# Kernel tuning notes

Hardware: AMD Instinct MI355X
Metric: run time of the kernel (lower is better)

## Reference

```python
import jax, jax.numpy as jnp
import numpy as np


def setup_inputs() -> dict:
    key = jax.random.key(0)
    ks = jax.random.split(key, 6)
    m, d, n, p = 4096, 1024, 16, 1024  # tokens, input_dim, num_experts, output_dim (=slots)
    h = (d + p) * 2 // 3  # 1365, hidden_dim per original module
    s = 0.02
    return {
        "x": jax.random.normal(ks[0], (m, d), jnp.float32),
        "phi": jax.random.normal(ks[1], (d, n, p), jnp.float32) * s,
        "W1": jax.random.normal(ks[2], (n, d, h), jnp.float32) * s,
        "b1": jax.random.normal(ks[3], (n, h), jnp.float32) * s,
        "W2": jax.random.normal(ks[4], (n, h, p), jnp.float32) * s,
        "b2": jax.random.normal(ks[5], (n, p), jnp.float32) * s,
    }


def reference(x, phi, W1, b1, W2, b2):
    # logits: [m, n, p] = tokens x experts x slots
    logits = jnp.einsum('md,dnp->mnp', x, phi)
    # Dispatch weights: softmax over tokens' expert axis (dim=1 in torch == experts n)
    D = jax.nn.softmax(logits, axis=1)
    # Combine weights: softmax over all (expert, slot) pairs per token
    m = logits.shape[0]
    C = jax.nn.softmax(logits.reshape(m, -1), axis=-1).reshape(logits.shape)
    # Slot inputs: [n, p, d]
    Xs = jnp.einsum('md,mnp->npd', x, D)
    # Batched per-expert MLP (replaces the Python loop over experts)
    H = jax.nn.relu(jnp.einsum('npd,ndh->nph', Xs, W1) + b1[:, None, :])
    Ys = jnp.einsum('nph,nho->npo', H, W2) + b2[:, None, :]  # [n, p, out]
    # Combine: [m, out]; flatten(start_dim=1) on a 2D tensor is a no-op
    Y = jnp.einsum('npo,mnp->mo', Ys, C)
    return Y
```

## Files before the change

### kernel.cpp

```cpp
#include <hip/hip_runtime.h>
#include <math.h>

#define MTOK 4096
#define DDIM 1024
#define NEXP 16
#define PSLOT 1024
#define NPDIM 16384
#define HDIM 1365
#define HPAD 1376
#define KSPL 4

typedef unsigned short u16;
typedef __attribute__((ext_vector_type(8))) short short8;
typedef __attribute__((ext_vector_type(8))) unsigned short ushort8;
typedef __attribute__((ext_vector_type(2))) unsigned int uint32x2;
typedef __attribute__((ext_vector_type(4))) unsigned int uint32x4;
typedef __attribute__((ext_vector_type(4))) float f32x4;

template<bool Bc, typename T, typename F> struct cond_t { using type = T; };
template<typename T, typename F> struct cond_t<false, T, F> { using type = F; };

__device__ __forceinline__ float b2f(u16 v) {
    union { unsigned int u; float f; } x;
    x.u = ((unsigned int)v) << 16;
    return x.f;
}
__device__ __forceinline__ u16 f2b(float f) {
    union { float f; unsigned int u; } x;
    x.f = f;
    unsigned int r = x.u + 0x7FFFu + ((x.u >> 16) & 1u);
    return (u16)(r >> 16);
}
__device__ __forceinline__ unsigned int cvtpk(float lo, float hi) {
    unsigned int r;
    asm("v_cvt_pk_bf16_f32 %0, %1, %2" : "=v"(r) : "v"(lo), "v"(hi));
    return r;
}
__device__ __forceinline__ void stv(float* p, long long i, float v) { p[i] = v; }
__device__ __forceinline__ void stv(u16*  p, long long i, float v) { p[i] = f2b(v); }

template<int AMODE, typename TA, typename TB, typename TC,
         bool BIASF, bool RELUF, bool ROWSC, bool BCHK>
__global__ __launch_bounds__(512) void mgemm(
    const TA* __restrict__ A, long long sA, int lda,
    const TB* __restrict__ B, long long sB, int ldb,
    TC* __restrict__ C, long long sC, int ldc,
    const float* __restrict__ S,
    const float* __restrict__ bias, long long sBias,
    const float* __restrict__ rowsc,
    int M, int N, int NZ, int K, int Kb, int Nb)
{
    constexpr int AS = (AMODE == 0) ? 32 : 40;
    constexpr int BS = 40;
    __shared__ u16 As[2][256 * AS];
    __shared__ u16 Bs[2][128 * BS];

    const int bz = blockIdx.z;
    A += (long long)bz * sA;
    B += (long long)bz * sB;
    C += (long long)bz * sC;
    const float* biasp = BIASF ? (bias + (long long)bz * sBias) : nullptr;

    const int gx = gridDim.x;
    const int nwg = gx * gridDim.y;
    int wg = blockIdx.x + gx * blockIdx.y;
    {
        const int q = nwg >> 3, r = nwg & 7, xc = wg & 7, ix = wg >> 3;
        wg = (xc < r ? xc * (q + 1) : r + xc * q) + ix;
    }
    const int m0 = (wg / gx) * 256;
    const int n0 = (wg % gx) * 128;

    const int tid  = threadIdx.x;
    const int lane = tid & 63;
    const int wv   = tid >> 6;
    const int wm   = wv & 3;
    const int wn   = wv >> 2;
    const int quad = lane >> 4;
    const int l16  = lane & 15;

    const int cla  = 2 * (tid & 127);
    const int k8a  = tid >> 7;
    const int clb  = 2 * (tid & 63);
    const int kqb  = tid >> 6;
    const int ngb  = n0 + clb;

    auto aoff = [&](int row, int k8) {
        int o = row * AS + k8 * 8;
        if constexpr (AMODE != 0) o ^= ((row >> 3) & 3) << 3;
        return o;
    };
    auto boff = [&](int row, int kel) {
        return (row * BS + kel) ^ (((row >> 3) & 3) << 3);
    };

    f32x4 acc[4][4];
#pragma unroll
    for (int i = 0; i < 4; ++i)
#pragma unroll
        for (int j = 0; j < 4; ++j) acc[i][j] = (f32x4){0.f, 0.f, 0.f, 0.f};

    using BRAW = typename cond_t<sizeof(TB) == 2, unsigned int[4], float[8]>::type;

    auto LOADA = [&](int k0, int buf, unsigned int (&araw)[8], float2 (&sr)[8]) {
        if constexpr (AMODE == 0) {
#pragma unroll
            for (int q = 0; q < 2; ++q) {
                const u16* gp = A + (long long)(m0 + wv * 32 + q * 16 + (lane >> 2)) * lda
                                  + k0 + (lane & 3) * 8;
                u16* lp = &As[buf][(wv * 32 + q * 16) * 32];
                __builtin_amdgcn_global_load_lds(
                    (const __attribute__((address_space(1))) unsigned int*)gp,
                    (__attribute__((address_space(3))) unsigned int*)lp, 16, 0, 0);
            }
        } else {
#pragma unroll
            for (int i = 0; i < 8; ++i) {
                const long long kg = k0 + k8a * 8 + i;
                araw[i] = *(const unsigned int*)((const u16*)A + kg * lda + (m0 + cla));
                sr[i]   = *(const float2*)&S[kg * 1024 + ((m0 + cla) & 1023)];
            }
        }
    };
    auto WRITEA = [&](int buf, unsigned int (&araw)[8], float2 (&sr)[8]) {
        if constexpr (AMODE != 0) {
            uint32x4 wa, wb;
#pragma unroll
            for (int j = 0; j < 4; ++j) {
                const unsigned int r0 = araw[2 * j], r1 = araw[2 * j + 1];
                wa[j] = cvtpk(b2f((u16)(r0 & 0xFFFFu)) * sr[2 * j].x,
                              b2f((u16)(r1 & 0xFFFFu)) * sr[2 * j + 1].x);
                wb[j] = cvtpk(b2f((u16)(r0 >> 16)) * sr[2 * j].y,
                              b2f((u16)(r1 >> 16)) * sr[2 * j + 1].y);
            }
            *(uint32x4*)&As[buf][aoff(cla, k8a)]     = wa;
            *(uint32x4*)&As[buf][aoff(cla + 1, k8a)] = wb;
        }
    };
    auto LOADB = [&](int k0, BRAW& braw) {
        if constexpr (sizeof(TB) == 2) {
#pragma unroll
            for (int i = 0; i < 4; ++i) {
                const int kg = k0 + kqb * 4 + i;
                braw[i] = *(const unsigned int*)((const u16*)B + (long long)kg * ldb + ngb);
            }
        } else {
            bool full = true;
            if constexpr (BCHK) full = (k0 + 32 <= Kb) && (n0 + 128 <= Nb);
            if (full) {
#pragma unroll
                for (int i = 0; i < 4; ++i) {
                    const int kg = k0 + kqb * 4 + i;
                    const float* bp = (const float*)B + (long long)kg * ldb + ngb;
                    braw[2 * i]     = bp[0];
                    braw[2 * i + 1] = bp[1];
                }
            } else {
#pragma unroll
                for (int i = 0; i < 4; ++i) {
                    const int kg = k0 + kqb * 4 + i;
                    float v0 = 0.f, v1 = 0.f;
                    if (kg < Kb) {
                        if (ngb < Nb)     v0 = ((const float*)B)[(long long)kg * ldb + ngb];
                        if (ngb + 1 < Nb) v1 = ((const float*)B)[(long long)kg * ldb + ngb + 1];
                    }
                    braw[2 * i]     = v0;
                    braw[2 * i + 1] = v1;
                }
            }
        }
    };
    auto WRITEB = [&](int buf, BRAW& braw) {
        uint32x2 wa, wb;
        if constexpr (sizeof(TB) == 2) {
            wa[0] = (braw[0] & 0xFFFFu) | (braw[1] << 16);
            wa[1] = (braw[2] & 0xFFFFu) | (braw[3] << 16);
            wb[0] = (braw[0] >> 16) | (braw[1] & 0xFFFF0000u);
            wb[1] = (braw[2] >> 16) | (braw[3] & 0xFFFF0000u);
        } else {
            wa[0] = cvtpk(braw[0], braw[2]);
            wa[1] = cvtpk(braw[4], braw[6]);
            wb[0] = cvtpk(braw[1], braw[3]);
            wb[1] = cvtpk(braw[5], braw[7]);
        }
        *(uint32x2*)&Bs[buf][boff(clb, kqb * 4)]     = wa;
        *(uint32x2*)&Bs[buf][boff(clb + 1, kqb * 4)] = wb;
    };
    auto MM = [&](int buf) {
        short8 bfr[4];
#pragma unroll
        for (int ni = 0; ni < 4; ++ni)
            bfr[ni] = *(const short8*)&Bs[buf][boff(wn * 64 + ni * 16 + l16, quad * 8)];
#pragma unroll
        for (int mi = 0; mi < 4; ++mi) {
            short8 a = *(const short8*)&As[buf][aoff(wm * 64 + mi * 16 + l16, quad)];
#pragma unroll
            for (int ni = 0; ni < 4; ++ni)
                acc[mi][ni] = __builtin_amdgcn_mfma_f32_16x16x32_bf16(a, bfr[ni], acc[mi][ni], 0, 0, 0);
        }
    };

    const int nt = K >> 5;
    {
        unsigned int araw[8];
        float2 sr[8];
        BRAW braw;
        LOADA(0, 0, araw, sr);
        LOADB(0, braw);
        WRITEA(0, araw, sr);
        WRITEB(0, braw);
        __syncthreads();
    }
    for (int t = 0; t < nt; ++t) {
        const int cur = t & 1, nxt = cur ^ 1;
        unsigned int araw[8];
        float2 sr[8];
        BRAW braw;
        const bool pf = (t + 1 < nt);
        if (pf) {
            LOADA((t + 1) * 32, nxt, araw, sr);
            LOADB((t + 1) * 32, braw);
        }
        MM(cur);
        if (pf) {
            WRITEA(nxt, araw, sr);
            WRITEB(nxt, braw);
        }
        __syncthreads();
    }

#pragma unroll
    for (int mi = 0; mi < 4; ++mi) {
#pragma unroll
        for (int r = 0; r < 4; ++r) {
            const int rg = m0 + wm * 64 + mi * 16 + quad * 4 + r;
            if (rg >= M) continue;
            const float rs = ROWSC ? rowsc[rg] : 1.f;
#pragma unroll
            for (int ni = 0; ni < 4; ++ni) {
                const int cg = n0 + wn * 64 + ni * 16 + l16;
                if (cg < N) {
                    float v = acc[mi][ni][r];
                    if (BIASF) v += biasp[cg];
                    if (RELUF) v = fmaxf(v, 0.f);
                    if (ROWSC) v *= rs;
                    stv(C, (long long)rg * ldc + cg, v);
                } else if (cg < NZ) {
                    stv(C, (long long)rg * ldc + cg, 0.f);
                }
            }
        }
    }
}

__global__ __launch_bounds__(256) void cvt_k(
    const float* __restrict__ src, u16* __restrict__ dst, long long n)
{
    const long long i = ((long long)blockIdx.x * 256 + threadIdx.x) * 8;
    if (i >= n) return;
    const float4 a = *(const float4*)&src[i];
    const float4 b = *(const float4*)&src[i + 4];
    uint32x4 v;
    v[0] = cvtpk(a.x, a.y);
    v[1] = cvtpk(a.z, a.w);
    v[2] = cvtpk(b.x, b.y);
    v[3] = cvtpk(b.z, b.w);
    *(uint32x4*)&dst[i] = v;
}

__global__ __launch_bounds__(256) void softmax_k(
    u16* __restrict__ L, float* __restrict__ rsd, float* __restrict__ rsc)
{
    const int m = blockIdx.x;
    u16* row = L + (long long)m * NPDIM;
    const int tid = threadIdx.x;
    __shared__ float red[256];

    float mx = -1e30f;
    for (int i = tid * 8; i < NPDIM; i += 2048) {
        const ushort8 v = *(const ushort8*)&row[i];
#pragma unroll
        for (int j = 0; j < 8; ++j) mx = fmaxf(mx, b2f(v[j]));
    }
    red[tid] = mx;
    __syncthreads();
    for (int s = 128; s > 0; s >>= 1) {
        if (tid < s) red[tid] = fmaxf(red[tid], red[tid + s]);
        __syncthreads();
    }
    const float mxAll = red[0];
    __syncthreads();

    float sum = 0.f;
    for (int i = tid * 8; i < NPDIM; i += 2048) {
        const ushort8 v = *(const ushort8*)&row[i];
        ushort8 e;
#pragma unroll
        for (int j = 0; j < 8; ++j) {
            const float ef = __expf(b2f(v[j]) - mxAll);
            const u16 eb = f2b(ef);
            e[j] = eb;
            sum += b2f(eb);
        }
        *(ushort8*)&row[i] = e;
    }
    red[tid] = sum;
    __syncthreads();
    for (int s = 128; s > 0; s >>= 1) {
        if (tid < s) red[tid] += red[tid + s];
        __syncthreads();
    }
    if (tid == 0) rsc[m] = 1.f / red[0];
    __syncthreads();

    {
        const int p0 = tid * 4;
        float s0 = 0.f, s1 = 0.f, s2 = 0.f, s3 = 0.f;
#pragma unroll
        for (int n = 0; n < NEXP; ++n) {
            const ushort4 v = *(const ushort4*)&row[n * PSLOT + p0];
            s0 += b2f(v.x); s1 += b2f(v.y); s2 += b2f(v.z); s3 += b2f(v.w);
        }
        const float4 r = {1.f / s0, 1.f / s1, 1.f / s2, 1.f / s3};
        *(float4*)&rsd[(long long)m * PSLOT + p0] = r;
    }
}

__global__ __launch_bounds__(256) void reduce_k(
    const float* __restrict__ Yp, float* __restrict__ Y)
{
    const long long S = (long long)MTOK * PSLOT;
    const long long i = ((long long)blockIdx.x * 256 + threadIdx.x) * 4;
    f32x4 r = *(const f32x4*)&Yp[i];
#pragma unroll
    for (int z = 1; z < KSPL; ++z) r += *(const f32x4*)&Yp[(long long)z * S + i];
    *(f32x4*)&Y[i] = r;
}

extern "C" void kernel_launch(void* const* d_in, const int* in_sizes, int n_in,
                              void* d_out, int out_size, void* d_ws, size_t ws_size,
                              hipStream_t stream)
{
    const float* x   = (const float*)d_in[0];
    const float* phi = (const float*)d_in[1];
    const float* W1  = (const float*)d_in[2];
    const float* b1  = (const float*)d_in[3];
    const float* W2  = (const float*)d_in[4];
    const float* b2  = (const float*)d_in[5];
    float* Y = (float*)d_out;

    char* w = (char*)d_ws;
    u16*   L    = (u16*)w;   w += (size_t)MTOK * NPDIM * 2;
    u16*   Ys   = (u16*)w;   w += (size_t)NEXP * PSLOT * PSLOT * 2;
    float* rsc  = (float*)w; w += (size_t)MTOK * 4;
    float* Yp   = (float*)w;
    float* rsd  = (float*)w; w += (size_t)MTOK * PSLOT * 4;
    u16*   Xs   = (u16*)w;   w += (size_t)NEXP * PSLOT * DDIM * 2;
    u16*   Hb   = (u16*)w;   w += (size_t)NEXP * PSLOT * HPAD * 2;
    u16*   phib = Ys;
    u16*   xb   = Hb;

    cvt_k<<<dim3((MTOK * DDIM) / (8 * 256)), 256, 0, stream>>>(x, xb, (long long)MTOK * DDIM);
    cvt_k<<<dim3((DDIM * NPDIM) / (8 * 256)), 256, 0, stream>>>(phi, phib, (long long)DDIM * NPDIM);

    mgemm<0, u16, u16, u16, false, false, false, false>
        <<<dim3(NPDIM / 128, MTOK / 256, 1), 512, 0, stream>>>(
        xb, 0, DDIM,  phib, 0, NPDIM,  L, 0, NPDIM,
        nullptr, nullptr, 0, nullptr,
        MTOK, NPDIM, NPDIM, DDIM, DDIM, NPDIM);

    softmax_k<<<dim3(MTOK), 256, 0, stream>>>(L, rsd, rsc);

    mgemm<2, u16, u16, u16, false, false, false, false>
        <<<dim3(DDIM / 128, NPDIM / 256, 1), 512, 0, stream>>>(
        L, 0, NPDIM,  xb, 0, DDIM,  Xs, 0, DDIM,
        rsd, nullptr, 0, nullptr,
        NPDIM, DDIM, DDIM, MTOK, MTOK, DDIM);

    mgemm<0, u16, float, u16, true, true, false, true>
        <<<dim3((HPAD + 127) / 128, PSLOT / 256, NEXP), 512, 0, stream>>>(
        Xs, (long long)PSLOT * DDIM, DDIM,
        W1, (long long)DDIM * HDIM, HDIM,
        Hb, (long long)PSLOT * HPAD, HPAD,
        nullptr, b1, HDIM, nullptr,
        PSLOT, HDIM, HPAD, DDIM, DDIM, HDIM);

    mgemm<0, u16, float, u16, true, false, false, true>
        <<<dim3(PSLOT / 128, PSLOT / 256, NEXP), 512, 0, stream>>>(
        Hb, (long long)PSLOT * HPAD, HPAD,
        W2, (long long)HDIM * PSLOT, PSLOT,
        Ys, (long long)PSLOT * PSLOT, PSLOT,
        nullptr, b2, PSLOT, nullptr,
        PSLOT, PSLOT, PSLOT, HPAD, HDIM, PSLOT);

    mgemm<0, u16, u16, float, false, false, true, false>
        <<<dim3(PSLOT / 128, MTOK / 256, KSPL), 512, 0, stream>>>(
        L, (long long)(NPDIM / KSPL), NPDIM,
        Ys, (long long)(NPDIM / KSPL) * PSLOT, PSLOT,
        Yp, (long long)MTOK * PSLOT, PSLOT,
        nullptr, nullptr, 0, rsc,
        MTOK, PSLOT, PSLOT, NPDIM / KSPL, NPDIM / KSPL, PSLOT);

    reduce_k<<<dim3((MTOK * PSLOT) / (4 * 256)), 256, 0, stream>>>(Yp, Y);
}
```

Measured before the change: 1.163 ms.

## Deepen GEMM register prefetch to two tiles ahead with manual waitcnt barriers

New measurement: 1.588 ms. +36.5%, slower.

```diff
diff --git a/kernel.cpp b/kernel.cpp
--- a/kernel.cpp
+++ b/kernel.cpp
@@ -38,6 +38,9 @@
 }
 __device__ __forceinline__ void stv(float* p, long long i, float v) { p[i] = v; }
 __device__ __forceinline__ void stv(u16*  p, long long i, float v) { p[i] = f2b(v); }
+
+#define BAR_LGKM()  asm volatile("s_waitcnt lgkmcnt(0)\ns_barrier" ::: "memory")
+#define BAR_VM(N)   asm volatile("s_waitcnt vmcnt(" #N ") lgkmcnt(0)\ns_barrier" ::: "memory")
 
 template<int AMODE, typename TA, typename TB, typename TC,
          bool BIASF, bool RELUF, bool ROWSC, bool BCHK>
@@ -102,40 +105,42 @@
 
     using BRAW = typename cond_t<sizeof(TB) == 2, unsigned int[4], float[8]>::type;
 
-    auto LOADA = [&](int k0, int buf, unsigned int (&araw)[8], float2 (&sr)[8]) {
-        if constexpr (AMODE == 0) {
-#pragma unroll
-            for (int q = 0; q < 2; ++q) {
-                const u16* gp = A + (long long)(m0 + wv * 32 + q * 16 + (lane >> 2)) * lda
-                                  + k0 + (lane & 3) * 8;
-                u16* lp = &As[buf][(wv * 32 + q * 16) * 32];
-                __builtin_amdgcn_global_load_lds(
-                    (const __attribute__((address_space(1))) unsigned int*)gp,
-                    (__attribute__((address_space(3))) unsigned int*)lp, 16, 0, 0);
-            }
-        } else {
-#pragma unroll
-            for (int i = 0; i < 8; ++i) {
-                const long long kg = k0 + k8a * 8 + i;
-                araw[i] = *(const unsigned int*)((const u16*)A + kg * lda + (m0 + cla));
-                sr[i]   = *(const float2*)&S[kg * 1024 + ((m0 + cla) & 1023)];
-            }
-        }
+    auto LOADA0 = [&](int k0, int buf) {
+#pragma unroll
+        for (int q = 0; q < 2; ++q) {
+            const u16* gp = A + (long long)(m0 + wv * 32 + q * 16 + (lane >> 2)) * lda
+                              + k0 + (lane & 3) * 8;
+            u16* lp = &As[buf][(wv * 32 + q * 16) * 32];
+            __builtin_amdgcn_global_load_lds(
+                (const __attribute__((address_space(1))) unsigned int*)gp,
+                (__attribute__((address_space(3))) unsigned int*)lp, 16, 0, 0);
+        }
+    };
+    auto LOADA2 = [&](int k0, unsigned int (&araw)[8]) {
+#pragma unroll
+        for (int i = 0; i < 8; ++i) {
+            const long long kg = k0 + k8a * 8 + i;
+            araw[i] = *(const unsigned int*)((const u16*)A + kg * lda + (m0 + cla));
+        }
+    };
+    auto LOADS = [&](int k0, float2 (&sr)[8]) {
+#pragma unroll
+        for (int i = 0; i < 8; ++i)
+            sr[i] = *(const float2*)&S[(long long)(k0 + k8a * 8 + i) * 1024
+                                       + ((m0 + cla) & 1023)];
     };
     auto WRITEA = [&](int buf, unsigned int (&araw)[8], float2 (&sr)[8]) {
-        if constexpr (AMODE != 0) {
-            uint32x4 wa, wb;
-#pragma unroll
-            for (int j = 0; j < 4; ++j) {
-                const unsigned int r0 = araw[2 * j], r1 = araw[2 * j + 1];
-                wa[j] = cvtpk(b2f((u16)(r0 & 0xFFFFu)) * sr[2 * j].x,
-                              b2f((u16)(r1 & 0xFFFFu)) * sr[2 * j + 1].x);
-                wb[j] = cvtpk(b2f((u16)(r0 >> 16)) * sr[2 * j].y,
-                              b2f((u16)(r1 >> 16)) * sr[2 * j + 1].y);
-            }
-            *(uint32x4*)&As[buf][aoff(cla, k8a)]     = wa;
-            *(uint32x4*)&As[buf][aoff(cla + 1, k8a)] = wb;
-        }
+        uint32x4 wa, wb;
+#pragma unroll
+        for (int j = 0; j < 4; ++j) {
+            const unsigned int r0 = araw[2 * j], r1 = araw[2 * j + 1];
+            wa[j] = cvtpk(b2f((u16)(r0 & 0xFFFFu)) * sr[2 * j].x,
+                          b2f((u16)(r1 & 0xFFFFu)) * sr[2 * j + 1].x);
+            wb[j] = cvtpk(b2f((u16)(r0 >> 16)) * sr[2 * j].y,
+                          b2f((u16)(r1 >> 16)) * sr[2 * j + 1].y);
+        }
+        *(uint32x4*)&As[buf][aoff(cla, k8a)]     = wa;
+        *(uint32x4*)&As[buf][aoff(cla + 1, k8a)] = wb;
     };
     auto LOADB = [&](int k0, BRAW& braw) {
         if constexpr (sizeof(TB) == 2) {
@@ -158,14 +163,15 @@
             } else {
 #pragma unroll
                 for (int i = 0; i < 4; ++i) {
-                    const int kg = k0 + kqb * 4 + i;
-                    float v0 = 0.f, v1 = 0.f;
-                    if (kg < Kb) {
-                        if (ngb < Nb)     v0 = ((const float*)B)[(long long)kg * ldb + ngb];
-                        if (ngb + 1 < Nb) v1 = ((const float*)B)[(long long)kg * ldb + ngb + 1];
-                    }
-                    braw[2 * i]     = v0;
-                    braw[2 * i + 1] = v1;
+                    const int kg  = k0 + kqb * 4 + i;
+                    const int kgc = kg < Kb ? kg : Kb - 1;
+                    const int c0  = ngb     < Nb ? ngb     : Nb - 1;
+                    const int c1  = ngb + 1 < Nb ? ngb + 1 : Nb - 1;
+                    const float* bp = (const float*)B + (long long)kgc * ldb;
+                    const float v0 = bp[c0];
+                    const float v1 = bp[c1];
+                    braw[2 * i]     = (kg < Kb && ngb     < Nb) ? v0 : 0.f;
+                    braw[2 * i + 1] = (kg < Kb && ngb + 1 < Nb) ? v1 : 0.f;
                 }
             }
         }
@@ -201,32 +207,46 @@
     };
 
     const int nt = K >> 5;
-    {
-        unsigned int araw[8];
-        float2 sr[8];
-        BRAW braw;
-        LOADA(0, 0, araw, sr);
-        LOADB(0, braw);
-        WRITEA(0, araw, sr);
-        WRITEB(0, braw);
-        __syncthreads();
-    }
-    for (int t = 0; t < nt; ++t) {
-        const int cur = t & 1, nxt = cur ^ 1;
-        unsigned int araw[8];
-        float2 sr[8];
-        BRAW braw;
-        const bool pf = (t + 1 < nt);
-        if (pf) {
-            LOADA((t + 1) * 32, nxt, araw, sr);
-            LOADB((t + 1) * 32, braw);
-        }
-        MM(cur);
-        if (pf) {
-            WRITEA(nxt, araw, sr);
-            WRITEB(nxt, braw);
-        }
-        __syncthreads();
+    unsigned int a0[8], a1[8];
+    BRAW b0, b1;
+    float2 sr[8];
+
+    auto STEP = [&](int t, unsigned int (&ha)[8], BRAW& hb,
+                    unsigned int (&na)[8], BRAW& nb) {
+        const int nxt = (t + 1) & 1;
+        const bool pf1 = (t + 1 < nt), pf2 = (t + 2 < nt);
+        if constexpr (AMODE == 0) {
+            if (pf1) LOADA0((t + 1) * 32, nxt);
+            __builtin_amdgcn_sched_barrier(0);
+            if (pf2) LOADB((t + 2) * 32, nb);
+            MM(t & 1);
+            if (pf1) WRITEB(nxt, hb);
+            if (pf2) { BAR_VM(4); } else { BAR_VM(0); }
+        } else {
+            if (pf1) LOADS((t + 1) * 32, sr);
+            if (pf2) { LOADA2((t + 2) * 32, na); LOADB((t + 2) * 32, nb); }
+            MM(t & 1);
+            if (pf1) { WRITEA(nxt, ha, sr); WRITEB(nxt, hb); }
+            BAR_LGKM();
+        }
+    };
+
+    if constexpr (AMODE == 0) {
+        LOADA0(0, 0);
+        __builtin_amdgcn_sched_barrier(0);
+        LOADB(0, b0);
+        WRITEB(0, b0);
+        LOADB(32, b1);
+        BAR_LGKM();
+    } else {
+        LOADA2(0, a0); LOADB(0, b0); LOADS(0, sr);
+        WRITEA(0, a0, sr); WRITEB(0, b0);
+        LOADA2(32, a1); LOADB(32, b1);
+        BAR_LGKM();
+    }
+    for (int t = 0; t < nt; t += 2) {
+        STEP(t, a1, b1, a0, b0);
+        if (t + 1 < nt) STEP(t + 1, a0, b0, a1, b1);
     }
 
 #pragma unroll
```

## Pre-transpose x and phi to bf16 so B tiles load directly into LDS

Applied to the files above, without the earlier changes.

After: 1.171 ms. No clear change (+0.6%).

```diff
diff --git a/kernel.cpp b/kernel.cpp
--- a/kernel.cpp
+++ b/kernel.cpp
@@ -39,7 +39,7 @@
 __device__ __forceinline__ void stv(float* p, long long i, float v) { p[i] = v; }
 __device__ __forceinline__ void stv(u16*  p, long long i, float v) { p[i] = f2b(v); }
 
-template<int AMODE, typename TA, typename TB, typename TC,
+template<int AMODE, int BMODE, typename TA, typename TB, typename TC,
          bool BIASF, bool RELUF, bool ROWSC, bool BCHK>
 __global__ __launch_bounds__(512) void mgemm(
     const TA* __restrict__ A, long long sA, int lda,
@@ -51,7 +51,7 @@
     int M, int N, int NZ, int K, int Kb, int Nb)
 {
     constexpr int AS = (AMODE == 0) ? 32 : 40;
-    constexpr int BS = 40;
+    constexpr int BS = (BMODE == 0) ? 32 : 40;
     __shared__ u16 As[2][256 * AS];
     __shared__ u16 Bs[2][128 * BS];
 
@@ -91,7 +91,9 @@
         return o;
     };
     auto boff = [&](int row, int kel) {
-        return (row * BS + kel) ^ (((row >> 3) & 3) << 3);
+        int o = row * BS + kel;
+        if constexpr (BMODE != 0) o ^= ((row >> 3) & 3) << 3;
+        return o;
     };
 
     f32x4 acc[4][4];
@@ -102,40 +104,45 @@
 
     using BRAW = typename cond_t<sizeof(TB) == 2, unsigned int[4], float[8]>::type;
 
-    auto LOADA = [&](int k0, int buf, unsigned int (&araw)[8], float2 (&sr)[8]) {
-        if constexpr (AMODE == 0) {
-#pragma unroll
-            for (int q = 0; q < 2; ++q) {
-                const u16* gp = A + (long long)(m0 + wv * 32 + q * 16 + (lane >> 2)) * lda
-                                  + k0 + (lane & 3) * 8;
-                u16* lp = &As[buf][(wv * 32 + q * 16) * 32];
-                __builtin_amdgcn_global_load_lds(
-                    (const __attribute__((address_space(1))) unsigned int*)gp,
-                    (__attribute__((address_space(3))) unsigned int*)lp, 16, 0, 0);
-            }
-        } else {
-#pragma unroll
-            for (int i = 0; i < 8; ++i) {
-                const long long kg = k0 + k8a * 8 + i;
-                araw[i] = *(const unsigned int*)((const u16*)A + kg * lda + (m0 + cla));
-                sr[i]   = *(const float2*)&S[kg * 1024 + ((m0 + cla) & 1023)];
-            }
+    auto LOADA0 = [&](int k0, int buf) {
+#pragma unroll
+        for (int q = 0; q < 2; ++q) {
+            const u16* gp = A + (long long)(m0 + wv * 32 + q * 16 + (lane >> 2)) * lda
+                              + k0 + (lane & 3) * 8;
+            u16* lp = &As[buf][(wv * 32 + q * 16) * 32];
+            __builtin_amdgcn_global_load_lds(
+                (const __attribute__((address_space(1))) unsigned int*)gp,
+                (__attribute__((address_space(3))) unsigned int*)lp, 16, 0, 0);
+        }
+    };
+    auto LOADA2 = [&](int k0, unsigned int (&araw)[8], float2 (&sr)[8]) {
+#pragma unroll
+        for (int i = 0; i < 8; ++i) {
+            const long long kg = k0 + k8a * 8 + i;
+            araw[i] = *(const unsigned int*)((const u16*)A + kg * lda + (m0 + cla));
+            sr[i]   = *(const float2*)&S[kg * 1024 + ((m0 + cla) & 1023)];
         }
     };
     auto WRITEA = [&](int buf, unsigned int (&araw)[8], float2 (&sr)[8]) {
-        if constexpr (AMODE != 0) {
-            uint32x4 wa, wb;
-#pragma unroll
-            for (int j = 0; j < 4; ++j) {
-                const unsigned int r0 = araw[2 * j], r1 = araw[2 * j + 1];
-                wa[j] = cvtpk(b2f((u16)(r0 & 0xFFFFu)) * sr[2 * j].x,
-                              b2f((u16)(r1 & 0xFFFFu)) * sr[2 * j + 1].x);
-                wb[j] = cvtpk(b2f((u16)(r0 >> 16)) * sr[2 * j].y,
-                              b2f((u16)(r1 >> 16)) * sr[2 * j + 1].y);
-            }
-            *(uint32x4*)&As[buf][aoff(cla, k8a)]     = wa;
-            *(uint32x4*)&As[buf][aoff(cla + 1, k8a)] = wb;
-        }
+        uint32x4 wa, wb;
+#pragma unroll
+        for (int j = 0; j < 4; ++j) {
+            const unsigned int r0 = araw[2 * j], r1 = araw[2 * j + 1];
+            wa[j] = cvtpk(b2f((u16)(r0 & 0xFFFFu)) * sr[2 * j].x,
+                          b2f((u16)(r1 & 0xFFFFu)) * sr[2 * j + 1].x);
+            wb[j] = cvtpk(b2f((u16)(r0 >> 16)) * sr[2 * j].y,
+                          b2f((u16)(r1 >> 16)) * sr[2 * j + 1].y);
+        }
+        *(uint32x4*)&As[buf][aoff(cla, k8a)]     = wa;
+        *(uint32x4*)&As[buf][aoff(cla + 1, k8a)] = wb;
+    };
+    auto LOADB0 = [&](int k0, int buf) {
+        const u16* gp = (const u16*)B + (long long)(n0 + wv * 16 + (lane >> 2)) * ldb
+                          + k0 + (lane & 3) * 8;
+        u16* lp = &Bs[buf][(wv * 16) * 32];
+        __builtin_amdgcn_global_load_lds(
+            (const __attribute__((address_space(1))) unsigned int*)gp,
+            (__attribute__((address_space(3))) unsigned int*)lp, 16, 0, 0);
     };
     auto LOADB = [&](int k0, BRAW& braw) {
         if constexpr (sizeof(TB) == 2) {
@@ -201,30 +208,31 @@
     };
 
     const int nt = K >> 5;
+    unsigned int a0[8];
+    float2 sr[8];
+    BRAW braw;
     {
-        unsigned int araw[8];
-        float2 sr[8];
-        BRAW braw;
-        LOADA(0, 0, araw, sr);
-        LOADB(0, braw);
-        WRITEA(0, araw, sr);
-        WRITEB(0, braw);
+        if constexpr (AMODE == 0) LOADA0(0, 0);
+        else                      LOADA2(0, a0, sr);
+        if constexpr (BMODE == 0) LOADB0(0, 0);
+        else                      LOADB(0, braw);
+        if constexpr (AMODE != 0) WRITEA(0, a0, sr);
+        if constexpr (BMODE != 0) WRITEB(0, braw);
         __syncthreads();
     }
     for (int t = 0; t < nt; ++t) {
         const int cur = t & 1, nxt = cur ^ 1;
-        unsigned int araw[8];
-        float2 sr[8];
-        BRAW braw;
         const bool pf = (t + 1 < nt);
         if (pf) {
-            LOADA((t + 1) * 32, nxt, araw, sr);
-            LOADB((t + 1) * 32, braw);
+            if constexpr (AMODE == 0) LOADA0((t + 1) * 32, nxt);
+            else                      LOADA2((t + 1) * 32, a0, sr);
+            if constexpr (BMODE == 0) LOADB0((t + 1) * 32, nxt);
+            else                      LOADB((t + 1) * 32, braw);
         }
         MM(cur);
         if (pf) {
-            WRITEA(nxt, araw, sr);
-            WRITEB(nxt, braw);
+            if constexpr (AMODE != 0) WRITEA(nxt, a0, sr);
+            if constexpr (BMODE != 0) WRITEB(nxt, braw);
         }
         __syncthreads();
     }
@@ -268,6 +276,25 @@
     *(uint32x4*)&dst[i] = v;
 }
 
+__global__ __launch_bounds__(256) void tcvt_k(
+    const float* __restrict__ src, u16* __restrict__ dst, int R, int C)
+{
+    __shared__ float t[32][33];
+    const int c0 = blockIdx.x * 32, r0 = blockIdx.y * 32;
+    const int tr = threadIdx.x >> 3;
+    const int tc = (threadIdx.x & 7) * 4;
+    const float4 v = *(const float4*)&src[(long long)(r0 + tr) * C + c0 + tc];
+    t[tr][tc]     = v.x;
+    t[tr][tc + 1] = v.y;
+    t[tr][tc + 2] = v.z;
+    t[tr][tc + 3] = v.w;
+    __syncthreads();
+    uint32x2 o;
+    o[0] = cvtpk(t[tc][tr],     t[tc + 1][tr]);
+    o[1] = cvtpk(t[tc + 2][tr], t[tc + 3][tr]);
+    *(uint32x2*)&dst[(long long)(c0 + tr) * R + r0 + tc] = o;
+}
+
 __global__ __launch_bounds__(256) void softmax_k(
     u16* __restrict__ L, float* __restrict__ rsd, float* __restrict__ rsc)
 {
@@ -350,34 +377,36 @@
     float* Y = (float*)d_out;
 
     char* w = (char*)d_ws;
-    u16*   L    = (u16*)w;   w += (size_t)MTOK * NPDIM * 2;
-    u16*   Ys   = (u16*)w;   w += (size_t)NEXP * PSLOT * PSLOT * 2;
-    float* rsc  = (float*)w; w += (size_t)MTOK * 4;
-    float* Yp   = (float*)w;
-    float* rsd  = (float*)w; w += (size_t)MTOK * PSLOT * 4;
-    u16*   Xs   = (u16*)w;   w += (size_t)NEXP * PSLOT * DDIM * 2;
-    u16*   Hb   = (u16*)w;   w += (size_t)NEXP * PSLOT * HPAD * 2;
-    u16*   phib = Ys;
-    u16*   xb   = Hb;
+    u16*   L     = (u16*)w;   w += (size_t)MTOK * NPDIM * 2;
+    u16*   Ys    = (u16*)w;   w += (size_t)NEXP * PSLOT * PSLOT * 2;
+    float* rsc   = (float*)w; w += (size_t)MTOK * 4;
+    float* Yp    = (float*)w;
+    float* rsd   = (float*)w; w += (size_t)MTOK * PSLOT * 4;
+    u16*   Xs    = (u16*)w;   w += (size_t)NEXP * PSLOT * DDIM * 2;
+    u16*   Hb    = (u16*)w;   w += (size_t)NEXP * PSLOT * HPAD * 2;
+    u16*   phibT = Ys;
+    u16*   xb    = Hb;
+    u16*   xbT   = Hb + (size_t)MTOK * DDIM;
 
     cvt_k<<<dim3((MTOK * DDIM) / (8 * 256)), 256, 0, stream>>>(x, xb, (long long)MTOK * DDIM);
-    cvt_k<<<dim3((DDIM * NPDIM) / (8 * 256)), 256, 0, stream>>>(phi, phib, (long long)DDIM * NPDIM);
-
-    mgemm<0, u16, u16, u16, false, false, false, false>
+    tcvt_k<<<dim3(DDIM / 32, MTOK / 32), 256, 0, stream>>>(x, xbT, MTOK, DDIM);
+    tcvt_k<<<dim3(NPDIM / 32, DDIM / 32), 256, 0, stream>>>(phi, phibT, DDIM, NPDIM);
+
+    mgemm<0, 0, u16, u16, u16, false, false, false, false>
         <<<dim3(NPDIM / 128, MTOK / 256, 1), 512, 0, stream>>>(
-        xb, 0, DDIM,  phib, 0, NPDIM,  L, 0, NPDIM,
+        xb, 0, DDIM,  phibT, 0, DDIM,  L, 0, NPDIM,
         nullptr, nullptr, 0, nullptr,
         MTOK, NPDIM, NPDIM, DDIM, DDIM, NPDIM);
 
     softmax_k<<<dim3(MTOK), 256, 0, stream>>>(L, rsd, rsc);
 
-    mgemm<2, u16, u16, u16, false, false, false, false>
+    mgemm<2, 0, u16, u16, u16, false, false, false, false>
         <<<dim3(DDIM / 128, NPDIM / 256, 1), 512, 0, stream>>>(
-        L, 0, NPDIM,  xb, 0, DDIM,  Xs, 0, DDIM,
+        L, 0, NPDIM,  xbT, 0, MTOK,  Xs, 0, DDIM,
         rsd, nullptr, 0, nullptr,
         NPDIM, DDIM, DDIM, MTOK, MTOK, DDIM);
 
-    mgemm<0, u16, float, u16, true, true, false, true>
+    mgemm<0, 1, u16, float, u16, true, true, false, true>
         <<<dim3((HPAD + 127) / 128, PSLOT / 256, NEXP), 512, 0, stream>>>(
         Xs, (long long)PSLOT * DDIM, DDIM,
         W1, (long long)DDIM * HDIM, HDIM,
@@ -385,7 +414,7 @@
         nullptr, b1, HDIM, nullptr,
         PSLOT, HDIM, HPAD, DDIM, DDIM, HDIM);
 
-    mgemm<0, u16, float, u16, true, false, false, true>
+    mgemm<0, 1, u16, float, u16, true, false, false, true>
         <<<dim3(PSLOT / 128, PSLOT / 256, NEXP), 512, 0, stream>>>(
         Hb, (long long)PSLOT * HPAD, HPAD,
         W2, (long long)HDIM * PSLOT, PSLOT,
@@ -393,7 +422,7 @@
         nullptr, b2, PSLOT, nullptr,
         PSLOT, PSLOT, PSLOT, HPAD, HDIM, PSLOT);
 
-    mgemm<0, u16, u16, float, false, false, true, false>
+    mgemm<0, 1, u16, u16, float, false, false, true, false>
         <<<dim3(PSLOT / 128, MTOK / 256, KSPL), 512, 0, stream>>>(
         L, (long long)(NPDIM / KSPL), NPDIM,
         Ys, (long long)(NPDIM / KSPL) * PSLOT, PSLOT,
```
